# Performance work log

Hardware: AMD Instinct MI355X
Metric: run time of the kernel (lower is better)

Reference implementation:

```python
import jax, jax.numpy as jnp
import numpy as np

B, T = 32, 4096
QD, MD, AD = 1024, 512, 128
F, K = 32, 31
PAD = (K - 1) // 2  # 'same' padding as in Tacotron-2 location conv


def setup_inputs() -> dict:
    key = jax.random.key(0)
    ks = jax.random.split(key, 12)
    s = lambda fan_in: 1.0 / np.sqrt(fan_in)
    return {
        "query": jax.random.normal(ks[0], (B, QD), jnp.float32),
        "memory": jax.random.normal(ks[1], (B, T, MD), jnp.float32),
        "alignments": jax.random.uniform(ks[2], (B, T, 2), jnp.float32),
        "mask": jnp.zeros((B, T), dtype=bool),
        "Wq": jax.random.normal(ks[3], (QD, AD), jnp.float32) * s(QD),
        "bq": jnp.zeros((AD,), jnp.float32),
        "Wm": jax.random.normal(ks[4], (MD, AD), jnp.float32) * s(MD),
        "bm": jnp.zeros((AD,), jnp.float32),
        "conv_w": jax.random.normal(ks[5], (F, 2, K), jnp.float32) * s(2 * K),
        "conv_b": jnp.zeros((F,), jnp.float32),
        "Wl": jax.random.normal(ks[6], (F, AD), jnp.float32) * s(F),
        "bl": jnp.zeros((AD,), jnp.float32),
        "v_w": jax.random.normal(ks[7], (AD,), jnp.float32) * s(AD),
        "v_b": jnp.zeros((), jnp.float32),
    }


def reference(query, memory, alignments, mask, Wq, bq, Wm, bm, conv_w, conv_b, Wl, bl, v_w, v_b):
    # processed memory: [B, T, AD]
    processed_memory = jnp.einsum("btm,ma->bta", memory, Wm) + bm
    # processed query: [B, 1, AD] (query.unsqueeze(1))
    processed_query = (query @ Wq + bq)[:, None, :]
    # location features: conv over time on [B, 2, T] -> [B, F, T]
    a = jnp.transpose(alignments, (0, 2, 1))  # [B, 2, T]
    loc = jax.lax.conv_general_dilated(
        a, conv_w, window_strides=(1,), padding=[(PAD, PAD)],
        dimension_numbers=("NCH", "OIH", "NCH"))
    loc = loc + conv_b[None, :, None]
    loc = jnp.transpose(loc, (0, 2, 1))  # [B, T, F]
    processed_loc = jnp.einsum("btf,fa->bta", loc, Wl) + bl
    # additive score: v . tanh(q + m + l)  -> [B, T]
    score = jnp.einsum("bta,a->bt", jnp.tanh(processed_query + processed_memory + processed_loc), v_w) + v_b
    score = jnp.where(mask, -jnp.inf, score)
    alignment = jax.nn.softmax(score, axis=-1)  # [B, T]
    context = jnp.einsum("bt,btm->bm", alignment, memory)  # [B, MD]
    return context, alignment
```

## Files before the change

### kernel.cpp

```cpp
#include <hip/hip_runtime.h>
#include <hip/hip_bf16.h>
#include <math.h>

#define B_ 32
#define T_ 4096
#define QD_ 1024
#define MD_ 512
#define AD_ 128
#define F_ 32
#define K_ 31
#define PAD_ 15

#define TT 64
#define NBLK (T_ / TT)

typedef float f32x16 __attribute__((ext_vector_type(16)));
typedef unsigned int uint4v __attribute__((ext_vector_type(4)));

__device__ inline unsigned pk_bf2(float lo, float hi) {
    unsigned ul = __float_as_uint(lo) + 0x8000u;
    unsigned uh = __float_as_uint(hi) + 0x8000u;
    return __builtin_amdgcn_perm(uh, ul, 0x07060302u);
}

__device__ inline unsigned short f2bf_rn(float f) {
    unsigned u = __float_as_uint(f);
    u += 0x7fffu + ((u >> 16) & 1u);
    return (unsigned short)(u >> 16);
}

__device__ inline float bf2f(unsigned short u) {
    return __uint_as_float(((unsigned)u) << 16);
}

__device__ inline void mfma32(f32x16& c, uint4v a, uint4v b) {
    asm("s_nop 1\n\tv_mfma_f32_32x32x16_bf16 %0, %1, %2, %0"
        : "+v"(c) : "v"(a), "v"(b));
}

__global__ __launch_bounds__(256) void k_prep(const float* __restrict__ Wm,
                                              unsigned short* __restrict__ wmT_sw) {
    int gid = blockIdx.x * 256 + threadIdx.x;
    int kk = gid >> 8;
    int ct = (gid >> 6) & 3;
    int lane = gid & 63;
    int k0 = kk * 16 + (lane >> 5) * 8;
    int a = ct * 32 + (lane & 31);
    unsigned short o[8];
#pragma unroll
    for (int j = 0; j < 8; j++) o[j] = f2bf_rn(Wm[(k0 + j) * AD_ + a]);
    uint4v v;
    v[0] = ((unsigned)o[1] << 16) | o[0];
    v[1] = ((unsigned)o[3] << 16) | o[2];
    v[2] = ((unsigned)o[5] << 16) | o[4];
    v[3] = ((unsigned)o[7] << 16) | o[6];
    *(uint4v*)(wmT_sw + (long)gid * 8) = v;
}

__global__ __launch_bounds__(128) void k_pq(const float* __restrict__ query,
                                            const float* __restrict__ Wq,
                                            float* __restrict__ pq) {
    int b = blockIdx.x;
    int qc = blockIdx.y;
    int a = threadIdx.x;
    const float* qrow = query + b * QD_ + qc * 128;
    const float* wq = Wq + (qc * 128) * AD_ + a;
    float acc = 0.f;
#pragma unroll 4
    for (int i = 0; i < 128; i++) acc += qrow[i] * wq[i * AD_];
    atomicAdd(&pq[b * AD_ + a], acc);
}

__global__ __launch_bounds__(256, 4) void k_score_ctx(
    const float* __restrict__ memory, const float* __restrict__ alignments,
    const unsigned char* __restrict__ mask,
    const unsigned short* __restrict__ wmT_sw, const float* __restrict__ bm,
    const float* __restrict__ convw, const float* __restrict__ convb,
    const float* __restrict__ Wl, const float* __restrict__ bl,
    const float* __restrict__ vw, const float* __restrict__ vb,
    const float* __restrict__ pq, const float* __restrict__ bq,
    float* __restrict__ scores, float* __restrict__ bmax,
    float* __restrict__ bden, float* __restrict__ num) {
    __shared__ __align__(16) unsigned short s_base[TT * AD_];
    __shared__ __align__(16) unsigned char s_u[16896];
    __shared__ float s_score[TT];
    __shared__ float s_w[TT];

    const int tid = threadIdx.x;
    const int b = blockIdx.y;
    const int blk = blockIdx.x;
    const int t0 = blk * TT;

    float* convw_s = (float*)s_u;
    float* align_s = convw_s + 1984;
    float* loc_s   = align_s + 192;
    unsigned short* sab = (unsigned short*)s_u;

    if (tid < TT) s_score[tid] = 0.f;

    for (int i = tid; i < F_ * 2 * K_; i += 256) convw_s[i] = convw[i];
    for (int i = tid; i < (TT + K_ - 1) * 2; i += 256) {
        int tg = t0 + (i >> 1) - PAD_;
        align_s[i] = (tg >= 0 && tg < T_) ? alignments[((long)b * T_ + tg) * 2 + (i & 1)] : 0.f;
    }
    __syncthreads();

    for (int i = tid; i < TT * F_; i += 256) {
        int f = i & (F_ - 1);
        int t = i >> 5;
        float acc = convb[f];
        const float* w0 = &convw_s[f * (2 * K_)];
        const float* w1 = w0 + K_;
        const float* al = &align_s[t * 2];
#pragma unroll
        for (int k = 0; k < K_; k++) acc += al[2 * k] * w0[k] + al[2 * k + 1] * w1[k];
        loc_s[t * F_ + f] = acc;
    }
    __syncthreads();

    for (int i = tid; i < TT * AD_; i += 256) {
        int a = i & (AD_ - 1);
        int t = i >> 7;
        float acc = pq[b * AD_ + a] + bq[a] + bm[a] + bl[a];
        const float* lrow = &loc_s[t * F_];
#pragma unroll
        for (int f = 0; f < F_; f++) acc += lrow[f] * Wl[f * AD_ + a];
        s_base[i] = f2bf_rn(acc);
    }
    __syncthreads();

    const int lane = tid & 63;
    const int w = tid >> 6;
    const int rt = w >> 1;
    const int ct0 = (w & 1) * 2;
    const int half = lane >> 5;
    const int l31 = lane & 31;

    const int srow = tid >> 3;
    const int skq = (tid & 7) * 4;
    const float* aptr = memory + ((long)b * T_ + t0) * MD_;
    const float* g_lo = aptr + srow * MD_ + skq;
    const float* g_hi = aptr + (srow + 32) * MD_ + skq;
    unsigned short* w_lo[2], * w_hi[2];
    w_lo[0] = sab + srow * 40 + skq;          w_hi[0] = sab + (srow + 32) * 40 + skq;
    w_lo[1] = w_lo[0] + 2560;                 w_hi[1] = w_hi[0] + 2560;

    const unsigned short* bptr = wmT_sw + ((long)ct0 * 64 + lane) * 8;
    const int arow = (rt * 32 + l31) * 40 + half * 8;

    f32x16 c0, c1;
#pragma unroll
    for (int i = 0; i < 16; i++) { c0[i] = 0.f; c1[i] = 0.f; }

    float4 A0 = *(const float4*)(g_lo);
    float4 A1 = *(const float4*)(g_hi);
    uint4v B00 = *(const uint4v*)(bptr);
    uint4v B01 = *(const uint4v*)(bptr + 512);
    uint4v B10 = *(const uint4v*)(bptr + 2048);
    uint4v B11 = *(const uint4v*)(bptr + 2048 + 512);
    ((unsigned*)w_lo[0])[0] = pk_bf2(A0.x, A0.y);
    ((unsigned*)w_lo[0])[1] = pk_bf2(A0.z, A0.w);
    ((unsigned*)w_hi[0])[0] = pk_bf2(A1.x, A1.y);
    ((unsigned*)w_hi[0])[1] = pk_bf2(A1.z, A1.w);
    __syncthreads();

    for (int c = 0; c < 16; c++) {
        const int cb = c & 1, nb = cb ^ 1;
        float4 N0, N1;
        uint4v NB00, NB01, NB10, NB11;
        {
            int kcn = (c < 15) ? (c + 1) * 32 : 0;
            N0 = *(const float4*)(g_lo + kcn);
            N1 = *(const float4*)(g_hi + kcn);
            long kkn = (c < 15) ? (long)(2 * c + 2) * 2048 : 0;
            NB00 = *(const uint4v*)(bptr + kkn);
            NB01 = *(const uint4v*)(bptr + kkn + 512);
            NB10 = *(const uint4v*)(bptr + kkn + 2048);
            NB11 = *(const uint4v*)(bptr + kkn + 2048 + 512);
        }
        uint4v af0 = *(const uint4v*)(sab + cb * 2560 + arow);
        uint4v af1 = *(const uint4v*)(sab + cb * 2560 + arow + 16);
        mfma32(c0, af0, B00);
        mfma32(c1, af0, B01);
        mfma32(c0, af1, B10);
        mfma32(c1, af1, B11);
        B00 = NB00; B01 = NB01; B10 = NB10; B11 = NB11;
        if (c < 15) {
            ((unsigned*)w_lo[nb])[0] = pk_bf2(N0.x, N0.y);
            ((unsigned*)w_lo[nb])[1] = pk_bf2(N0.z, N0.w);
            ((unsigned*)w_hi[nb])[0] = pk_bf2(N1.x, N1.y);
            ((unsigned*)w_hi[nb])[1] = pk_bf2(N1.z, N1.w);
        }
        __syncthreads();
    }
    asm volatile("s_nop 7\n\ts_nop 7\n\ts_nop 7" ::: "memory");

    float vwa0 = vw[ct0 * 32 + l31];
    float vwa1 = vw[ct0 * 32 + 32 + l31];
#pragma unroll
    for (int i = 0; i < 16; i++) {
        int t = rt * 32 + (i & 3) + 8 * (i >> 2) + 4 * half;
        float b0 = bf2f(s_base[t * AD_ + ct0 * 32 + l31]);
        float b1 = bf2f(s_base[t * AD_ + ct0 * 32 + 32 + l31]);
        float s = tanhf(c0[i] + b0) * vwa0 + tanhf(c1[i] + b1) * vwa1;
        s += __shfl_xor(s, 1);
        s += __shfl_xor(s, 2);
        s += __shfl_xor(s, 4);
        s += __shfl_xor(s, 8);
        s += __shfl_xor(s, 16);
        if (l31 == 0) atomicAdd(&s_score[t], s);
    }
    __syncthreads();

    if (tid < TT) {
        float s = s_score[tid] + vb[0];
        bool mk = mask[(long)b * T_ + t0 + tid] != 0;
        if (mk) s = -INFINITY;
        scores[b * T_ + t0 + tid] = s;
        float m = s;
#pragma unroll
        for (int off = 32; off >= 1; off >>= 1) m = fmaxf(m, __shfl_xor(m, off));
        float e = (m == -INFINITY) ? 0.f : expf(s - m);
        float d = e;
#pragma unroll
        for (int off = 32; off >= 1; off >>= 1) d += __shfl_xor(d, off);
        s_w[tid] = e;
        if (tid == 0) {
            bmax[b * NBLK + blk] = m;
            bden[b * NBLK + blk] = d;
        }
    }
    __syncthreads();

    {
        const float2* mp = (const float2*)aptr + tid;
        float ax = 0.f, ay = 0.f;
#pragma unroll 8
        for (int t = 0; t < TT; t++) {
            float2 v = mp[t * 256];
            float wt = s_w[t];
            ax += wt * v.x;
            ay += wt * v.y;
        }
        float2 o; o.x = ax; o.y = ay;
        *(float2*)(num + ((long)b * NBLK + blk) * MD_ + tid * 2) = o;
    }
}

__global__ __launch_bounds__(512) void k_reduce(
    const float* __restrict__ bmax, const float* __restrict__ bden,
    const float* __restrict__ num, const float* __restrict__ scores,
    float* __restrict__ ctx, float* __restrict__ oalign) {
    int b = blockIdx.x;
    int tid = threadIdx.x;
    __shared__ float sm[NBLK], se[NBLK];
    __shared__ float sD;
    if (tid < NBLK) sm[tid] = bmax[b * NBLK + tid];
    __syncthreads();
    float M = -INFINITY;
#pragma unroll
    for (int i = 0; i < NBLK; i++) M = fmaxf(M, sm[i]);
    if (tid < NBLK) se[tid] = expf(sm[tid] - M) * bden[b * NBLK + tid];
    __syncthreads();
    if (tid == 0) {
        float D = 0.f;
        for (int i = 0; i < NBLK; i++) D += se[i];
        sD = D;
    }
    if (tid < NBLK) se[tid] = expf(sm[tid] - M);
    __syncthreads();
    float invD = 1.f / sD;

    float acc = 0.f;
    const float* np = num + (long)b * NBLK * MD_ + tid;
#pragma unroll 8
    for (int blk = 0; blk < NBLK; blk++) acc += se[blk] * np[blk * MD_];
    ctx[b * MD_ + tid] = acc * invD;

    for (int t = tid; t < T_; t += 512) {
        oalign[b * T_ + t] = expf(scores[b * T_ + t] - M) * invD;
    }
}

extern "C" void kernel_launch(void* const* d_in, const int* in_sizes, int n_in,
                              void* d_out, int out_size, void* d_ws, size_t ws_size,
                              hipStream_t stream) {
    const float* query      = (const float*)d_in[0];
    const float* memory     = (const float*)d_in[1];
    const float* alignments = (const float*)d_in[2];
    const unsigned char* mask = (const unsigned char*)d_in[3];
    const float* Wq    = (const float*)d_in[4];
    const float* bq    = (const float*)d_in[5];
    const float* Wm    = (const float*)d_in[6];
    const float* bm    = (const float*)d_in[7];
    const float* convw = (const float*)d_in[8];
    const float* convb = (const float*)d_in[9];
    const float* Wl    = (const float*)d_in[10];
    const float* bl    = (const float*)d_in[11];
    const float* vw    = (const float*)d_in[12];
    const float* vb    = (const float*)d_in[13];

    float* out = (float*)d_out;
    float* ctx = out;
    float* oalign = out + B_ * MD_;

    float* ws = (float*)d_ws;
    float* pq     = ws;
    float* scores = pq + B_ * AD_;
    float* bmax   = scores + B_ * T_;
    float* bden   = bmax + B_ * NBLK;
    float* num    = bden + B_ * NBLK;
    unsigned short* wmT_sw = (unsigned short*)(num + (long)B_ * NBLK * MD_);

    hipMemsetAsync(pq, 0, B_ * AD_ * sizeof(float), stream);

    k_prep<<<32, 256, 0, stream>>>(Wm, wmT_sw);
    k_pq<<<dim3(B_, QD_ / 128), 128, 0, stream>>>(query, Wq, pq);
    k_score_ctx<<<dim3(NBLK, B_), 256, 0, stream>>>(
        memory, alignments, mask, wmT_sw, bm, convw, convb, Wl, bl, vw, vb, pq, bq,
        scores, bmax, bden, num);
    k_reduce<<<B_, 512, 0, stream>>>(bmax, bden, num, scores, ctx, oalign);
}
```

Measured before the change: 485.5 us.

## Restructure score kernel: 128-row tiles, direct-register A operands, fast tanh/exp

Doubles the time tile to 128 rows so each wave owns 32 rows and all 128 attention columns. A fragments now go straight from global memory into registers, which removes the LDS staging and the per-chunk barriers of the MFMA loop. Also restructures the conv and Wl projection loops for register reuse, swaps tanhf/expf for exp-based fast approximations, and adds a missing barrier in the reduce kernel. This raises register and LDS use per block (launch bounds lowered to 3) and reduces the number of blocks, and the approximations slightly change accuracy.

```diff
diff --git a/kernel.cpp b/kernel.cpp
--- a/kernel.cpp
+++ b/kernel.cpp
@@ -11,7 +11,7 @@
 #define K_ 31
 #define PAD_ 15
 
-#define TT 64
+#define TT 128
 #define NBLK (T_ / TT)
 
 typedef float f32x16 __attribute__((ext_vector_type(16)));
@@ -36,6 +36,11 @@
 __device__ inline void mfma32(f32x16& c, uint4v a, uint4v b) {
     asm("s_nop 1\n\tv_mfma_f32_32x32x16_bf16 %0, %1, %2, %0"
         : "+v"(c) : "v"(a), "v"(b));
+}
+
+__device__ inline float fast_tanh(float x) {
+    float e = __expf(2.f * x);
+    return 1.f - 2.f / (e + 1.f);
 }
 
 __global__ __launch_bounds__(256) void k_prep(const float* __restrict__ Wm,
@@ -71,7 +76,7 @@
     atomicAdd(&pq[b * AD_ + a], acc);
 }
 
-__global__ __launch_bounds__(256, 4) void k_score_ctx(
+__global__ __launch_bounds__(256, 3) void k_score_ctx(
     const float* __restrict__ memory, const float* __restrict__ alignments,
     const unsigned char* __restrict__ mask,
     const unsigned short* __restrict__ wmT_sw, const float* __restrict__ bm,
@@ -82,7 +87,8 @@
     float* __restrict__ scores, float* __restrict__ bmax,
     float* __restrict__ bden, float* __restrict__ num) {
     __shared__ __align__(16) unsigned short s_base[TT * AD_];
-    __shared__ __align__(16) unsigned char s_u[16896];
+    __shared__ __align__(16) float s_loc[TT * F_];
+    __shared__ __align__(16) float s_align[(TT + K_ - 1) * 2 + 2];
     __shared__ float s_score[TT];
     __shared__ float s_w[TT];
 
@@ -91,140 +97,170 @@
     const int blk = blockIdx.x;
     const int t0 = blk * TT;
 
-    float* convw_s = (float*)s_u;
-    float* align_s = convw_s + 1984;
-    float* loc_s   = align_s + 192;
-    unsigned short* sab = (unsigned short*)s_u;
-
-    if (tid < TT) s_score[tid] = 0.f;
-
-    for (int i = tid; i < F_ * 2 * K_; i += 256) convw_s[i] = convw[i];
+    const int lane = tid & 63;
+    const int w = tid >> 6;
+    const int half = lane >> 5;
+    const int l31 = lane & 31;
+
+    const float* aRow = memory + ((long)(b * T_ + t0 + w * 32 + l31)) * MD_ + half * 8;
+    float4 p00 = *(const float4*)(aRow + 0);
+    float4 p01 = *(const float4*)(aRow + 4);
+    float4 p02 = *(const float4*)(aRow + 16);
+    float4 p03 = *(const float4*)(aRow + 20);
+    float4 p10 = *(const float4*)(aRow + 32);
+    float4 p11 = *(const float4*)(aRow + 36);
+    float4 p12 = *(const float4*)(aRow + 48);
+    float4 p13 = *(const float4*)(aRow + 52);
+
     for (int i = tid; i < (TT + K_ - 1) * 2; i += 256) {
         int tg = t0 + (i >> 1) - PAD_;
-        align_s[i] = (tg >= 0 && tg < T_) ? alignments[((long)b * T_ + tg) * 2 + (i & 1)] : 0.f;
-    }
-    __syncthreads();
-
-    for (int i = tid; i < TT * F_; i += 256) {
-        int f = i & (F_ - 1);
-        int t = i >> 5;
-        float acc = convb[f];
-        const float* w0 = &convw_s[f * (2 * K_)];
+        s_align[i] = (tg >= 0 && tg < T_) ? alignments[((long)b * T_ + tg) * 2 + (i & 1)] : 0.f;
+    }
+    __syncthreads();
+
+    {
+        const int f = tid & 31;
+        const int tg = tid >> 5;
+        float accv[16];
+        float cb = convb[f];
+#pragma unroll
+        for (int j = 0; j < 16; j++) accv[j] = cb;
+        const float* w0 = convw + f * (2 * K_);
         const float* w1 = w0 + K_;
-        const float* al = &align_s[t * 2];
-#pragma unroll
-        for (int k = 0; k < K_; k++) acc += al[2 * k] * w0[k] + al[2 * k + 1] * w1[k];
-        loc_s[t * F_ + f] = acc;
-    }
-    __syncthreads();
-
-    for (int i = tid; i < TT * AD_; i += 256) {
-        int a = i & (AD_ - 1);
-        int t = i >> 7;
-        float acc = pq[b * AD_ + a] + bq[a] + bm[a] + bl[a];
-        const float* lrow = &loc_s[t * F_];
-#pragma unroll
-        for (int f = 0; f < F_; f++) acc += lrow[f] * Wl[f * AD_ + a];
-        s_base[i] = f2bf_rn(acc);
-    }
-    __syncthreads();
-
-    const int lane = tid & 63;
-    const int w = tid >> 6;
-    const int rt = w >> 1;
-    const int ct0 = (w & 1) * 2;
-    const int half = lane >> 5;
-    const int l31 = lane & 31;
-
-    const int srow = tid >> 3;
-    const int skq = (tid & 7) * 4;
-    const float* aptr = memory + ((long)b * T_ + t0) * MD_;
-    const float* g_lo = aptr + srow * MD_ + skq;
-    const float* g_hi = aptr + (srow + 32) * MD_ + skq;
-    unsigned short* w_lo[2], * w_hi[2];
-    w_lo[0] = sab + srow * 40 + skq;          w_hi[0] = sab + (srow + 32) * 40 + skq;
-    w_lo[1] = w_lo[0] + 2560;                 w_hi[1] = w_hi[0] + 2560;
-
-    const unsigned short* bptr = wmT_sw + ((long)ct0 * 64 + lane) * 8;
-    const int arow = (rt * 32 + l31) * 40 + half * 8;
-
-    f32x16 c0, c1;
-#pragma unroll
-    for (int i = 0; i < 16; i++) { c0[i] = 0.f; c1[i] = 0.f; }
-
-    float4 A0 = *(const float4*)(g_lo);
-    float4 A1 = *(const float4*)(g_hi);
-    uint4v B00 = *(const uint4v*)(bptr);
-    uint4v B01 = *(const uint4v*)(bptr + 512);
-    uint4v B10 = *(const uint4v*)(bptr + 2048);
-    uint4v B11 = *(const uint4v*)(bptr + 2048 + 512);
-    ((unsigned*)w_lo[0])[0] = pk_bf2(A0.x, A0.y);
-    ((unsigned*)w_lo[0])[1] = pk_bf2(A0.z, A0.w);
-    ((unsigned*)w_hi[0])[0] = pk_bf2(A1.x, A1.y);
-    ((unsigned*)w_hi[0])[1] = pk_bf2(A1.z, A1.w);
-    __syncthreads();
-
-    for (int c = 0; c < 16; c++) {
-        const int cb = c & 1, nb = cb ^ 1;
-        float4 N0, N1;
-        uint4v NB00, NB01, NB10, NB11;
+        for (int k = 0; k < K_; k++) {
+            float wa = w0[k], wb = w1[k];
+            const float2* al = (const float2*)&s_align[0] + (tg * 16 + k);
+#pragma unroll
+            for (int j = 0; j < 16; j++) {
+                float2 v = al[j];
+                accv[j] += v.x * wa + v.y * wb;
+            }
+        }
+#pragma unroll
+        for (int j = 0; j < 16; j++) s_loc[(tg * 16 + j) * F_ + f] = accv[j];
+    }
+    __syncthreads();
+
+    {
+        const int a = tid & 127;
+        float cbase = pq[b * AD_ + a] + bq[a] + bm[a] + bl[a];
+        float wl[32];
+#pragma unroll
+        for (int f = 0; f < 32; f++) wl[f] = Wl[f * AD_ + a];
+        for (int jj = 0; jj < 64; jj++) {
+            int t = (tid >> 7) + jj * 2;
+            const float4* lr = (const float4*)&s_loc[t * F_];
+            float racc = cbase;
+#pragma unroll
+            for (int f4 = 0; f4 < 8; f4++) {
+                float4 lv = lr[f4];
+                racc += lv.x * wl[f4 * 4] + lv.y * wl[f4 * 4 + 1]
+                      + lv.z * wl[f4 * 4 + 2] + lv.w * wl[f4 * 4 + 3];
+            }
+            s_base[t * AD_ + a] = f2bf_rn(racc);
+        }
+    }
+    __syncthreads();
+
+    const unsigned short* bp = wmT_sw + (long)lane * 8;
+
+    f32x16 c0, c1, c2, c3;
+#pragma unroll
+    for (int i = 0; i < 16; i++) { c0[i] = 0.f; c1[i] = 0.f; c2[i] = 0.f; c3[i] = 0.f; }
+
+#pragma unroll 2
+    for (int c = 0; c < 16; c += 2) {
         {
-            int kcn = (c < 15) ? (c + 1) * 32 : 0;
-            N0 = *(const float4*)(g_lo + kcn);
-            N1 = *(const float4*)(g_hi + kcn);
-            long kkn = (c < 15) ? (long)(2 * c + 2) * 2048 : 0;
-            NB00 = *(const uint4v*)(bptr + kkn);
-            NB01 = *(const uint4v*)(bptr + kkn + 512);
-            NB10 = *(const uint4v*)(bptr + kkn + 2048);
-            NB11 = *(const uint4v*)(bptr + kkn + 2048 + 512);
-        }
-        uint4v af0 = *(const uint4v*)(sab + cb * 2560 + arow);
-        uint4v af1 = *(const uint4v*)(sab + cb * 2560 + arow + 16);
-        mfma32(c0, af0, B00);
-        mfma32(c1, af0, B01);
-        mfma32(c0, af1, B10);
-        mfma32(c1, af1, B11);
-        B00 = NB00; B01 = NB01; B10 = NB10; B11 = NB11;
-        if (c < 15) {
-            ((unsigned*)w_lo[nb])[0] = pk_bf2(N0.x, N0.y);
-            ((unsigned*)w_lo[nb])[1] = pk_bf2(N0.z, N0.w);
-            ((unsigned*)w_hi[nb])[0] = pk_bf2(N1.x, N1.y);
-            ((unsigned*)w_hi[nb])[1] = pk_bf2(N1.z, N1.w);
-        }
-        __syncthreads();
+            uint4v af0, af1;
+            af0[0] = pk_bf2(p00.x, p00.y); af0[1] = pk_bf2(p00.z, p00.w);
+            af0[2] = pk_bf2(p01.x, p01.y); af0[3] = pk_bf2(p01.z, p01.w);
+            af1[0] = pk_bf2(p02.x, p02.y); af1[1] = pk_bf2(p02.z, p02.w);
+            af1[2] = pk_bf2(p03.x, p03.y); af1[3] = pk_bf2(p03.z, p03.w);
+            int kc = (c + 2 < 16) ? (c + 2) * 32 : 0;
+            p00 = *(const float4*)(aRow + kc);
+            p01 = *(const float4*)(aRow + kc + 4);
+            p02 = *(const float4*)(aRow + kc + 16);
+            p03 = *(const float4*)(aRow + kc + 20);
+            const unsigned short* bb = bp + (long)(8 * c) * 512;
+            uint4v B00 = *(const uint4v*)(bb);
+            uint4v B01 = *(const uint4v*)(bb + 512);
+            uint4v B02 = *(const uint4v*)(bb + 1024);
+            uint4v B03 = *(const uint4v*)(bb + 1536);
+            uint4v B10 = *(const uint4v*)(bb + 2048);
+            uint4v B11 = *(const uint4v*)(bb + 2560);
+            uint4v B12 = *(const uint4v*)(bb + 3072);
+            uint4v B13 = *(const uint4v*)(bb + 3584);
+            mfma32(c0, af0, B00); mfma32(c1, af0, B01);
+            mfma32(c2, af0, B02); mfma32(c3, af0, B03);
+            mfma32(c0, af1, B10); mfma32(c1, af1, B11);
+            mfma32(c2, af1, B12); mfma32(c3, af1, B13);
+        }
+        {
+            uint4v af0, af1;
+            af0[0] = pk_bf2(p10.x, p10.y); af0[1] = pk_bf2(p10.z, p10.w);
+            af0[2] = pk_bf2(p11.x, p11.y); af0[3] = pk_bf2(p11.z, p11.w);
+            af1[0] = pk_bf2(p12.x, p12.y); af1[1] = pk_bf2(p12.z, p12.w);
+            af1[2] = pk_bf2(p13.x, p13.y); af1[3] = pk_bf2(p13.z, p13.w);
+            int kc = (c + 3 < 16) ? (c + 3) * 32 : 0;
+            p10 = *(const float4*)(aRow + kc);
+            p11 = *(const float4*)(aRow + kc + 4);
+            p12 = *(const float4*)(aRow + kc + 16);
+            p13 = *(const float4*)(aRow + kc + 20);
+            const unsigned short* bb = bp + (long)(8 * c + 8) * 512;
+            uint4v B00 = *(const uint4v*)(bb);
+            uint4v B01 = *(const uint4v*)(bb + 512);
+            uint4v B02 = *(const uint4v*)(bb + 1024);
+            uint4v B03 = *(const uint4v*)(bb + 1536);
+            uint4v B10 = *(const uint4v*)(bb + 2048);
+            uint4v B11 = *(const uint4v*)(bb + 2560);
+            uint4v B12 = *(const uint4v*)(bb + 3072);
+            uint4v B13 = *(const uint4v*)(bb + 3584);
+            mfma32(c0, af0, B00); mfma32(c1, af0, B01);
+            mfma32(c2, af0, B02); mfma32(c3, af0, B03);
+            mfma32(c0, af1, B10); mfma32(c1, af1, B11);
+            mfma32(c2, af1, B12); mfma32(c3, af1, B13);
+        }
     }
     asm volatile("s_nop 7\n\ts_nop 7\n\ts_nop 7" ::: "memory");
 
-    float vwa0 = vw[ct0 * 32 + l31];
-    float vwa1 = vw[ct0 * 32 + 32 + l31];
-#pragma unroll
-    for (int i = 0; i < 16; i++) {
-        int t = rt * 32 + (i & 3) + 8 * (i >> 2) + 4 * half;
-        float b0 = bf2f(s_base[t * AD_ + ct0 * 32 + l31]);
-        float b1 = bf2f(s_base[t * AD_ + ct0 * 32 + 32 + l31]);
-        float s = tanhf(c0[i] + b0) * vwa0 + tanhf(c1[i] + b1) * vwa1;
-        s += __shfl_xor(s, 1);
-        s += __shfl_xor(s, 2);
-        s += __shfl_xor(s, 4);
-        s += __shfl_xor(s, 8);
-        s += __shfl_xor(s, 16);
-        if (l31 == 0) atomicAdd(&s_score[t], s);
-    }
-    __syncthreads();
-
-    if (tid < TT) {
-        float s = s_score[tid] + vb[0];
-        bool mk = mask[(long)b * T_ + t0 + tid] != 0;
-        if (mk) s = -INFINITY;
-        scores[b * T_ + t0 + tid] = s;
-        float m = s;
+    {
+        float vw0 = vw[l31], vw1 = vw[32 + l31], vw2 = vw[64 + l31], vw3 = vw[96 + l31];
+#pragma unroll
+        for (int i = 0; i < 16; i++) {
+            int rl = (i & 3) + 8 * (i >> 2) + 4 * half;
+            int r = w * 32 + rl;
+            const unsigned short* br = &s_base[r * AD_ + l31];
+            float s = fast_tanh(c0[i] + bf2f(br[0]))   * vw0
+                    + fast_tanh(c1[i] + bf2f(br[32]))  * vw1
+                    + fast_tanh(c2[i] + bf2f(br[64]))  * vw2
+                    + fast_tanh(c3[i] + bf2f(br[96]))  * vw3;
+            s += __shfl_xor(s, 1);
+            s += __shfl_xor(s, 2);
+            s += __shfl_xor(s, 4);
+            s += __shfl_xor(s, 8);
+            s += __shfl_xor(s, 16);
+            if (l31 == 0) s_score[r] = s;
+        }
+    }
+    __syncthreads();
+
+    if (tid < 64) {
+        float s0v = s_score[tid] + vb[0];
+        float s1v = s_score[tid + 64] + vb[0];
+        if (mask[(long)b * T_ + t0 + tid]) s0v = -INFINITY;
+        if (mask[(long)b * T_ + t0 + 64 + tid]) s1v = -INFINITY;
+        scores[b * T_ + t0 + tid] = s0v;
+        scores[b * T_ + t0 + 64 + tid] = s1v;
+        float m = fmaxf(s0v, s1v);
 #pragma unroll
         for (int off = 32; off >= 1; off >>= 1) m = fmaxf(m, __shfl_xor(m, off));
-        float e = (m == -INFINITY) ? 0.f : expf(s - m);
-        float d = e;
+        float e0 = (m == -INFINITY) ? 0.f : __expf(s0v - m);
+        float e1 = (m == -INFINITY) ? 0.f : __expf(s1v - m);
+        float d = e0 + e1;
 #pragma unroll
         for (int off = 32; off >= 1; off >>= 1) d += __shfl_xor(d, off);
-        s_w[tid] = e;
+        s_w[tid] = e0;
+        s_w[tid + 64] = e1;
         if (tid == 0) {
             bmax[b * NBLK + blk] = m;
             bden[b * NBLK + blk] = d;
@@ -233,11 +269,11 @@
     __syncthreads();
 
     {
-        const float2* mp = (const float2*)aptr + tid;
+        const float2* mp = (const float2*)(memory + ((long)b * T_ + t0) * MD_) + tid;
         float ax = 0.f, ay = 0.f;
 #pragma unroll 8
         for (int t = 0; t < TT; t++) {
-            float2 v = mp[t * 256];
+            float2 v = mp[(long)t * 256];
             float wt = s_w[t];
             ax += wt * v.x;
             ay += wt * v.y;
@@ -260,14 +296,15 @@
     float M = -INFINITY;
 #pragma unroll
     for (int i = 0; i < NBLK; i++) M = fmaxf(M, sm[i]);
-    if (tid < NBLK) se[tid] = expf(sm[tid] - M) * bden[b * NBLK + tid];
+    if (tid < NBLK) se[tid] = __expf(sm[tid] - M) * bden[b * NBLK + tid];
     __syncthreads();
     if (tid == 0) {
         float D = 0.f;
         for (int i = 0; i < NBLK; i++) D += se[i];
         sD = D;
     }
-    if (tid < NBLK) se[tid] = expf(sm[tid] - M);
+    __syncthreads();
+    if (tid < NBLK) se[tid] = __expf(sm[tid] - M);
     __syncthreads();
     float invD = 1.f / sD;
 
@@ -278,7 +315,7 @@
     ctx[b * MD_ + tid] = acc * invD;
 
     for (int t = tid; t < T_; t += 512) {
-        oalign[b * T_ + t] = expf(scores[b * T_ + t] - M) * invD;
+        oalign[b * T_ + t] = __expf(scores[b * T_ + t] - M) * invD;
     }
 }
 
```

Measured after the change: 499.6 us. 2.9% more time.
